# Optimization experiments

Hardware: AMD Instinct MI355X
Metric: run time of the kernel (lower is better)

Reference implementation:

```python
import jax, jax.numpy as jnp
import numpy as np

NUM_WORDS = 10000
IN_DIM = 300
SIZE = 256
NUM_SEQ = 2
B = 16
L = 128
NUM_BASE_LEMMAS = 3000


def _lstm(x, Wi, Wh, b):
    # x: [L, B, D] -> hidden states [L, B, H]
    Bb = x.shape[1]
    H = Wh.shape[0]
    def step(carry, xt):
        h, c = carry
        z = xt @ Wi + h @ Wh + b  # [B, 4H], gate order i,f,g,o (torch convention)
        i, f, g, o = jnp.split(z, 4, axis=-1)
        c = jax.nn.sigmoid(f) * c + jax.nn.sigmoid(i) * jnp.tanh(g)
        h = jax.nn.sigmoid(o) * jnp.tanh(c)
        return (h, c), h
    init = (jnp.zeros((Bb, H), x.dtype), jnp.zeros((Bb, H), x.dtype))
    _, hs = jax.lax.scan(step, init, x)
    return hs


def _bilstm(x, lengths, Wi_f, Wh_f, b_f, Wi_b, Wh_b, b_b):
    # x: [B, L, D]; variable-length bidirectional LSTM, concat outputs [B, L, 2H]
    Bb, Ll, _ = x.shape
    t = jnp.arange(Ll)
    # reverse the valid prefix of each row; padding stays in place
    rev_idx = jnp.where(t[None, :] < lengths[:, None], lengths[:, None] - 1 - t[None, :], t[None, :])
    x_rev = jnp.take_along_axis(x, rev_idx[:, :, None], axis=1)
    hf = _lstm(jnp.swapaxes(x, 0, 1), Wi_f, Wh_f, b_f)
    hb = _lstm(jnp.swapaxes(x_rev, 0, 1), Wi_b, Wh_b, b_b)
    hf = jnp.swapaxes(hf, 0, 1)
    hb = jnp.take_along_axis(jnp.swapaxes(hb, 0, 1), rev_idx[:, :, None], axis=1)
    return jnp.concatenate([hf, hb], axis=-1)


def setup_inputs() -> dict:
    key = jax.random.key(0)
    ks = jax.random.split(key, 16)
    d = {}
    d['word_embeddings'] = jax.random.normal(ks[0], (NUM_WORDS, IN_DIM), jnp.float32)
    # embedding projection Linear(IN_DIM, SIZE)
    d['Wp'] = jax.random.normal(ks[1], (IN_DIM, SIZE), jnp.float32) * 0.05
    d['bp'] = jnp.zeros((SIZE,), jnp.float32)
    D = SIZE + NUM_SEQ
    d['Wi_f'] = jax.random.normal(ks[2], (D, 4 * SIZE), jnp.float32) * 0.05
    d['Wh_f'] = jax.random.normal(ks[3], (SIZE, 4 * SIZE), jnp.float32) * 0.05
    d['b_f'] = jnp.zeros((4 * SIZE,), jnp.float32)
    d['Wi_b'] = jax.random.normal(ks[4], (D, 4 * SIZE), jnp.float32) * 0.05
    d['Wh_b'] = jax.random.normal(ks[5], (SIZE, 4 * SIZE), jnp.float32) * 0.05
    d['b_b'] = jnp.zeros((4 * SIZE,), jnp.float32)
    # encoded projection Linear(2*SIZE, SIZE)
    d['Wenc'] = jax.random.normal(ks[6], (2 * SIZE, SIZE), jnp.float32) * 0.05
    d['benc'] = jnp.zeros((SIZE,), jnp.float32)
    # gate projection Linear(2*SIZE, SIZE), bias init 1.0 per source
    d['Wgate'] = jax.random.normal(ks[7], (2 * SIZE, SIZE), jnp.float32) * 0.05
    d['bgate'] = jnp.ones((SIZE,), jnp.float32)
    d['seq0'] = jax.random.randint(ks[8], (B, L), 0, NUM_WORDS, jnp.int32)
    d['seq1'] = jax.random.randint(ks[9], (B, L), 0, NUM_WORDS, jnp.int32)
    d['len0'] = jax.random.randint(ks[10], (B,), 1, L + 1, jnp.int32)
    d['len1'] = jax.random.randint(ks[11], (B,), 1, L + 1, jnp.int32)
    d['u2l'] = jax.random.randint(ks[12], (NUM_WORDS,), 0, NUM_BASE_LEMMAS, jnp.int32)
    return d


def reference(word_embeddings, Wp, bp, Wi_f, Wh_f, b_f, Wi_b, Wh_b, b_b, Wenc, benc, Wgate, bgate, seq0, seq1, len0, len1, u2l):
    num_words = word_embeddings.shape[0]
    batch = seq0.shape[0]
    size = Wp.shape[1]
    we = jax.nn.relu(word_embeddings @ Wp + bp)  # [num_words, size]
    offsets = jnp.arange(batch, dtype=jnp.int32) * num_words  # [B]
    u2l_off = (u2l[None, :] + offsets[:, None]).reshape(-1)  # [B*num_words]
    num_lemmas = batch * num_words
    ctxt = jnp.tile(we, (batch, 1))  # [B*num_words, size]
    for i, (seq, lengths) in enumerate(((seq0, len0), (seq1, len1))):
        Ll = seq.shape[1]
        seq_off = seq + offsets[:, None]  # [B, L]
        enc_in = ctxt[seq_off]  # gather: [B, L, size]
        mode = jnp.zeros((batch, Ll, NUM_SEQ), enc_in.dtype).at[:, :, i].set(1.0)
        enc_in = jnp.concatenate([enc_in, mode], axis=-1)  # [B, L, size+num_seq]
        h = _bilstm(enc_in, lengths, Wi_f, Wh_f, b_f, Wi_b, Wh_b, b_b)  # [B, L, 2*size]
        enc = h @ Wenc + benc  # [B, L, size]
        mask = (jnp.arange(Ll)[None, :] < lengths[:, None]).astype(enc.dtype)
        enc = enc * mask[:, :, None]
        seq_lemmas = u2l_off[seq_off.reshape(-1)]  # [B*L]
        new_lemma = jax.ops.segment_max(enc.reshape(-1, size), seq_lemmas, num_segments=num_lemmas)
        new_lemma = jax.nn.relu(new_lemma)  # empty segments (-inf) -> 0
        new_word = new_lemma[u2l_off]  # scatter-back via gather: [B*num_words, size]
        gate = jax.nn.sigmoid(jnp.concatenate([ctxt, new_word], axis=-1) @ Wgate + bgate)
        ctxt = ctxt * gate + (1.0 - gate) * new_word
    return ctxt
```

## Files before the change

kernel.cpp:

```cpp
#include <hip/hip_runtime.h>

#define NW    10000
#define INDIM 300
#define SZ    256
#define BB    16
#define LL    128
#define NLEM  3000
#define FH    1024
#define NCAP  8192

typedef short  bf16x8 __attribute__((ext_vector_type(8)));
typedef float  f32x4  __attribute__((ext_vector_type(4)));

__device__ __forceinline__ float sigf(float x){
  return __builtin_amdgcn_rcpf(1.f+__builtin_amdgcn_exp2f(-1.442695041f*x));
}
__device__ __forceinline__ float tanhf_(float x){
  return fmaf(-2.f, __builtin_amdgcn_rcpf(1.f+__builtin_amdgcn_exp2f(2.885390082f*x)), 1.f);
}
__device__ __forceinline__ short f2b(float f){
  unsigned u=__float_as_uint(f); u += 0x7FFFu + ((u>>16)&1u); return (short)(u>>16);
}
__device__ __forceinline__ int pack2(float a, float b){
  return ((int)(unsigned short)f2b(a)) | (((int)(unsigned short)f2b(b))<<16);
}
#define B2F(s) __uint_as_float(((unsigned)(unsigned short)(s))<<16)
#define MFA(a,b,c) __builtin_amdgcn_mfma_f32_16x16x32_bf16(a,b,c,0,0,0)

__global__ void k_we(const float* __restrict__ emb, const float* __restrict__ Wp,
                     const float* __restrict__ bp, float* __restrict__ we){
  __shared__ __align__(16) float As[16][INDIM];
  int r0 = blockIdx.x*16, tid = threadIdx.x;
  for(int i=tid;i<16*INDIM;i+=256){int lr=i/INDIM,d=i-lr*INDIM;
    As[lr][d]=emb[(long)(r0+lr)*INDIM+d];}
  __syncthreads();
  int cl=tid&63, rg=tid>>6;
  float acc[4][4];
  #pragma unroll
  for(int i=0;i<4;i++){acc[i][0]=acc[i][1]=acc[i][2]=acc[i][3]=0.f;}
  for(int k=0;k<INDIM;k+=4){
    float4 a4[4];
    #pragma unroll
    for(int i=0;i<4;i++) a4[i]=*(const float4*)&As[rg*4+i][k];
    #pragma unroll
    for(int j=0;j<4;j++){
      const float* wr=Wp+(long)(k+j)*SZ+cl;
      float w0=wr[0],w1=wr[64],w2=wr[128],w3=wr[192];
      #pragma unroll
      for(int i=0;i<4;i++){
        float a=(j==0)?a4[i].x:(j==1)?a4[i].y:(j==2)?a4[i].z:a4[i].w;
        acc[i][0]=fmaf(a,w0,acc[i][0]);acc[i][1]=fmaf(a,w1,acc[i][1]);
        acc[i][2]=fmaf(a,w2,acc[i][2]);acc[i][3]=fmaf(a,w3,acc[i][3]);
      }
    }
  }
  #pragma unroll
  for(int i=0;i<4;i++){
    int r=r0+rg*4+i;
    #pragma unroll
    for(int cc=0;cc<4;cc++){int col=cl+cc*64;
      we[(long)r*SZ+col]=fmaxf(acc[i][cc]+bp[col],0.f);}
  }
}

__global__ void k_prep(const float* __restrict__ Wh_f, const float* __restrict__ Wh_b,
                       short* __restrict__ frag){
  int tid = blockIdx.x*256 + threadIdx.x;
  int l=tid&63, f=(tid>>6)&63, w=(tid>>12)&7, dir=tid>>15;
  const float* Wh = dir? Wh_b : Wh_f;
  int ks=f&7, T2=f>>3, s2=T2>>2, g=T2&3;
  int col = g*256 + w*32 + s2*16 + (l&15);
  int k0  = ks*32 + (l>>4)*8;
  short v[8];
  #pragma unroll
  for(int j=0;j<8;j++) v[j]=f2b(Wh[(long)(k0+j)*FH + col]);
  *(bf16x8*)(frag + (long)tid*8) = *(bf16x8*)v;
}

__global__ void k_prepwi(const float* __restrict__ Wi_f, const float* __restrict__ Wi_b,
                         short* __restrict__ wf){
  int tid = blockIdx.x*256 + threadIdx.x;
  int l=tid&63, ks=(tid>>6)&7, ct=(tid>>9)&63, dir=tid>>15;
  const float* Wi = dir? Wi_b : Wi_f;
  int col = ct*16 + (l&15);
  int k0  = ks*32 + (l>>4)*8;
  short v[8];
  #pragma unroll
  for(int j=0;j<8;j++) v[j]=f2b(Wi[(long)(k0+j)*FH + col]);
  *(bf16x8*)(wf + (long)tid*8) = *(bf16x8*)v;
}

__global__ void k_prepenc(const float* __restrict__ Wenc, short* __restrict__ wef){
  int tid = blockIdx.x*256 + threadIdx.x;
  int l=tid&63, ks=(tid>>6)&15, ct=tid>>10;
  int col = ct*16 + (l&15);
  int k0  = ks*32 + (l>>4)*8;
  short v[8];
  #pragma unroll
  for(int j=0;j<8;j++) v[j]=f2b(Wenc[(long)(k0+j)*SZ + col]);
  *(bf16x8*)(wef + (long)tid*8) = *(bf16x8*)v;
}

__global__ void k_xwi_mfma(const int* __restrict__ seq, const int* __restrict__ len,
                      const float* __restrict__ srcw, long bstride,
                      const float* __restrict__ ctxtT, const int* __restrict__ idxmap,
                      const float* __restrict__ Wi_f, const float* __restrict__ bvf,
                      const float* __restrict__ Wi_b, const float* __restrict__ bvb,
                      const short* __restrict__ wf, int iseq, short* __restrict__ xwo){
  __shared__ __align__(16) short As[64*264];
  __shared__ const float* rowp[64];
  int bx=blockIdx.x, dir=bx>>5, blk=bx&31, tid=threadIdx.x;
  int w=tid>>6, l=tid&63;
  if(tid<64){
    int t = blk*4 + (tid>>4), b = tid&15;
    int lb=len[b];
    int tt=(dir==0)? t : ((t<lb)? (lb-1-t) : t);
    int tok=seq[b*LL+tt];
    const float* rp;
    if(idxmap){
      int im=idxmap[b*NW+tok];
      rp = (im>=0)? ctxtT+(long)im*SZ : srcw+(long)tok*SZ;
    }else{
      rp = srcw + (long)b*bstride + (long)tok*SZ;
    }
    rowp[tid]=rp;
  }
  __syncthreads();
  for(int i2=tid;i2<64*64;i2+=256){
    int lr=i2>>6, c4=(i2&63)*4;
    float4 v=*(const float4*)(rowp[lr]+c4);
    int2 pk; pk.x=pack2(v.x,v.y); pk.y=pack2(v.z,v.w);
    *(int2*)&As[lr*264+c4]=pk;
  }
  __syncthreads();
  const float* __restrict__ Wi = dir? Wi_b : Wi_f;
  const float* __restrict__ bv = dir? bvb : bvf;
  const short* wfd = wf + (long)dir*262144;
  for(int n2=0;n2<16;n2++){
    int ct = w*16 + n2;
    const short* bfp = wfd + ((long)ct*8)*512 + l*8;
    f32x4 Z={0.f,0.f,0.f,0.f};
    f32x4 C0=Z,C1=Z,C2=Z,C3=Z;
    #pragma unroll
    for(int ks=0;ks<8;ks++){
      bf16x8 bb=*(const bf16x8*)(bfp + ks*512);
      int ao = ks*32 + (l>>4)*8;
      bf16x8 a0=*(const bf16x8*)(&As[((l&15)    )*264 + ao]);
      bf16x8 a1=*(const bf16x8*)(&As[((l&15)+16 )*264 + ao]);
      bf16x8 a2=*(const bf16x8*)(&As[((l&15)+32 )*264 + ao]);
      bf16x8 a3=*(const bf16x8*)(&As[((l&15)+48 )*264 + ao]);
      C0=MFA(a0,bb,C0); C1=MFA(a1,bb,C1); C2=MFA(a2,bb,C2); C3=MFA(a3,bb,C3);
    }
    int g=ct>>4, w2=(ct&15)>>1, s2=ct&1;
    int col = g*256 + w2*32 + s2*16 + (l&15);
    float be = Wi[(long)(SZ+iseq)*FH+col] + bv[col];
    #pragma unroll
    for(int m=0;m<4;m++){
      f32x4 Cm = (m==0)?C0:(m==1)?C1:(m==2)?C2:C3;
      long base=((((long)dir*128 + blk*4 + m)*8 + w2)*64 + (l>>4)*16 + (l&15))*32
                + s2*16 + g*4;
      int2 pk; pk.x=pack2(Cm[0]+be,Cm[1]+be); pk.y=pack2(Cm[2]+be,Cm[3]+be);
      *(int2*)(xwo+base)=pk;
    }
  }
}

#define LDFW(f)    (*(const bf16x8*)(fr + (long)(f)*512 + l*8))
#define LDLW(i2,ks) (*(const bf16x8*)(bl + ((i2)*8+(ks))*512 + l*8))
#define DECLWT(T) bf16x8 W##T##_0=LDFW((T)*8+0),W##T##_1=LDFW((T)*8+1),W##T##_2=LDFW((T)*8+2),W##T##_3=LDFW((T)*8+3),W##T##_4=LDFW((T)*8+4),W##T##_5=LDFW((T)*8+5),W##T##_6=LDFW((T)*8+6),W##T##_7=LDFW((T)*8+7);
#define MMRT(T,Cv) { Cv=MFA(A0,W##T##_0,Cv); Cv=MFA(A1,W##T##_1,Cv); Cv=MFA(A2,W##T##_2,Cv); Cv=MFA(A3,W##T##_3,Cv); Cv=MFA(A4,W##T##_4,Cv); Cv=MFA(A5,W##T##_5,Cv); Cv=MFA(A6,W##T##_6,Cv); Cv=MFA(A7,W##T##_7,Cv); }
#define MMLT(i2,Cv) { Cv=MFA(A0,LDLW(i2,0),Cv); Cv=MFA(A1,LDLW(i2,1),Cv); Cv=MFA(A2,LDLW(i2,2),Cv); Cv=MFA(A3,LDLW(i2,3),Cv); Cv=MFA(A4,LDLW(i2,4),Cv); Cv=MFA(A5,LDLW(i2,5),Cv); Cv=MFA(A6,LDLW(i2,6),Cv); Cv=MFA(A7,LDLW(i2,7),Cv); }
#define MMST(Cv) { Cv=MFA(A0,S0,Cv); Cv=MFA(A1,S1,Cv); Cv=MFA(A2,S2,Cv); Cv=MFA(A3,S3,Cv); Cv=MFA(A4,S4,Cv); Cv=MFA(A5,S5,Cv); Cv=MFA(A6,S6,Cv); Cv=MFA(A7,S7,Cv); }
#define LOADST(f0) S0=LDFW((f0)+0); S1=LDFW((f0)+1); S2=LDFW((f0)+2); S3=LDFW((f0)+3); S4=LDFW((f0)+4); S5=LDFW((f0)+5); S6=LDFW((f0)+6); S7=LDFW((f0)+7);
#define G1(s,r,CA,CB,CC,CD,XA,XB) { \
  float zi=CA[r]+B2F(XA[r]), zf=CB[r]+B2F(XA[4+(r)]), zg=CC[r]+B2F(XB[r]), zo=CD[r]+B2F(XB[4+(r)]); \
  cst_##s##_##r = sigf(zf)*cst_##s##_##r + sigf(zi)*tanhf_(zg); \
  float hv = sigf(zo)*tanhf_(cst_##s##_##r); \
  int b_=4*(l>>4)+(r); int u_=w*32+(s)*16+(l&15); \
  hbn[b_*264+u_]=f2b(hv); }
#define GP(s,CA,CB,CC,CD,XA,XB) \
  G1(s,0,CA,CB,CC,CD,XA,XB) G1(s,1,CA,CB,CC,CD,XA,XB) \
  G1(s,2,CA,CB,CC,CD,XA,XB) G1(s,3,CA,CB,CC,CD,XA,XB)

extern __shared__ char smem_raw[];

__global__ __launch_bounds__(512,2) void k_lstm_w8(
    const short* __restrict__ frag, const short* __restrict__ xq,
    short* __restrict__ hgs){
  const int dir=blockIdx.x, tid=threadIdx.x, w=tid>>6, l=tid&63;
  short* hb=(short*)smem_raw;
  short* bl=(short*)(smem_raw+16896)+w*8192;
  const short* fr = frag + (long)(dir*8+w)*32768;
  for(int i=tid;i<4224;i+=512) ((int*)smem_raw)[i]=0;
  #pragma unroll
  for(int c2=0;c2<16;c2++)
    *(f32x4*)(bl+c2*512+l*8) = *(const f32x4*)(fr+(long)(32+c2)*512+l*8);
  DECLWT(0) DECLWT(1) DECLWT(2) DECLWT(3)
  float cst_0_0=0,cst_0_1=0,cst_0_2=0,cst_0_3=0,
        cst_1_0=0,cst_1_1=0,cst_1_2=0,cst_1_3=0;
  __syncthreads();
  const short* xwb = xq + ((long)dir*128*8 + w)*2048 + (long)l*32;
  short* hgb = hgs + (long)dir*524288;
  const int db=tid>>5, du=(tid&31)*8;
  bf16x8 S0,S1,S2,S3,S4,S5,S6,S7;
  for(int t=0;t<LL;t++){
    const int cur=t&1, nxt=cur^1;
    LOADST(48)
    const short* xp = xwb + (long)t*16384;
    bf16x8 X0=*(const bf16x8*)(xp+0), X1=*(const bf16x8*)(xp+8);
    const short* hr = hb + cur*4224 + (l&15)*264 + (l>>4)*8;
    bf16x8 A0=*(const bf16x8*)(hr+0),   A1=*(const bf16x8*)(hr+32),
           A2=*(const bf16x8*)(hr+64),  A3=*(const bf16x8*)(hr+96),
           A4=*(const bf16x8*)(hr+128), A5=*(const bf16x8*)(hr+160),
           A6=*(const bf16x8*)(hr+192), A7=*(const bf16x8*)(hr+224);
    f32x4 Z={0.f,0.f,0.f,0.f};
    f32x4 C00=Z,C01=Z,C02=Z,C03=Z,C10=Z,C11=Z,C12=Z,C13=Z;
    MMRT(0,C00) MMRT(1,C01) MMRT(2,C02) MMRT(3,C03)
    MMLT(0,C10) MMLT(1,C11)
    MMST(C12)
    LOADST(56)
    bf16x8 X2=*(const bf16x8*)(xp+16), X3=*(const bf16x8*)(xp+24);
    short* hbn = hb + nxt*4224;
    GP(0, C00,C01,C02,C03, X0,X1)
    MMST(C13)
    GP(1, C10,C11,C12,C13, X2,X3)
    __syncthreads();
    f32x4 hv4 = *(const f32x4*)(hbn + db*264 + du);
    *(f32x4*)(hgb + ((long)t*16 + db)*256 + du) = hv4;
  }
}

__global__ void k_enc_mfma(const int* __restrict__ seq, const int* __restrict__ len,
                      const int* __restrict__ u2l, const short* __restrict__ hgs,
                      const short* __restrict__ wef, const float* __restrict__ benc,
                      unsigned int* __restrict__ lembuf, unsigned int* __restrict__ flags){
  __shared__ __align__(16) short As[64*520];
  __shared__ const short* pf16[64]; __shared__ const short* pb16[64];
  __shared__ int lem_s[64], val_s[64], b_s[64];
  int r0=blockIdx.x*64, tid=threadIdx.x, w=tid>>6, l=tid&63;
  if(tid<64){
    int r=r0+tid, b=r>>7, t=r&127, lb=len[b];
    int v=(t<lb); val_s[tid]=v; b_s[tid]=b;
    int lem=u2l[seq[r]]; lem_s[tid]=lem;
    pf16[tid]=hgs+((long)t*BB+b)*SZ;
    int tr=v? (lb-1-t) : t;
    pb16[tid]=hgs+((long)(LL+tr)*BB+b)*SZ;
    if(v) flags[(long)b*NLEM+lem]=1u;
  }
  __syncthreads();
  for(int i2=tid;i2<64*128;i2+=256){
    int lr=i2>>7, cc=(i2&127)*4;
    const short* sp=(cc<256)? pf16[lr]+cc : pb16[lr]+(cc-256);
    *(int2*)&As[lr*520+cc]=*(const int2*)sp;
  }
  __syncthreads();
  for(int n2=0;n2<4;n2++){
    int ct=w*4+n2;
    f32x4 Z={0.f,0.f,0.f,0.f};
    f32x4 C0=Z,C1=Z,C2=Z,C3=Z;
    #pragma unroll
    for(int ks=0;ks<16;ks++){
      bf16x8 bb=*(const bf16x8*)(wef+((long)(ct*16+ks))*512+l*8);
      int ao=ks*32+(l>>4)*8;
      bf16x8 a0=*(const bf16x8*)(&As[((l&15)    )*520+ao]);
      bf16x8 a1=*(const bf16x8*)(&As[((l&15)+16 )*520+ao]);
      bf16x8 a2=*(const bf16x8*)(&As[((l&15)+32 )*520+ao]);
      bf16x8 a3=*(const bf16x8*)(&As[((l&15)+48 )*520+ao]);
      C0=MFA(a0,bb,C0); C1=MFA(a1,bb,C1); C2=MFA(a2,bb,C2); C3=MFA(a3,bb,C3);
    }
    int col=ct*16+(l&15);
    float be=benc[col];
    #pragma unroll
    for(int m=0;m<4;m++){
      f32x4 Cm=(m==0)?C0:(m==1)?C1:(m==2)?C2:C3;
      #pragma unroll
      for(int reg=0;reg<4;reg++){
        int row=m*16+(l>>4)*4+reg;
        if(val_s[row]){
          float e=fmaxf(Cm[reg]+be,0.f);
          atomicMax(&lembuf[((long)b_s[row]*NLEM+lem_s[row])*SZ+col], __float_as_uint(e));
        }
      }
    }
  }
}

__global__ void k_rowgemm(const float* __restrict__ A, const float* __restrict__ W,
                          float* __restrict__ C, const unsigned int* __restrict__ flags){
  __shared__ __align__(16) float As[16][SZ];
  __shared__ int any_s;
  int r0=blockIdx.x*16, tid=threadIdx.x;
  if(tid==0){
    int a = flags? 0 : 1;
    if(flags){ for(int i=0;i<16;i++) a |= (int)flags[r0+i]; }
    any_s=a;
  }
  __syncthreads();
  if(!any_s) return;
  for(int i=tid;i<16*SZ;i+=256){int lr=i>>8,j=i&(SZ-1);As[lr][j]=A[(long)(r0+lr)*SZ+j];}
  __syncthreads();
  int cl=tid&63, rg=tid>>6;
  float acc[4][4];
  #pragma unroll
  for(int i=0;i<4;i++){acc[i][0]=acc[i][1]=acc[i][2]=acc[i][3]=0.f;}
  for(int k=0;k<SZ;k+=4){
    float4 a4[4];
    #pragma unroll
    for(int i=0;i<4;i++) a4[i]=*(const float4*)&As[rg*4+i][k];
    #pragma unroll
    for(int j=0;j<4;j++){
      const float* wr=W+(long)(k+j)*SZ+cl;
      float w0=wr[0],w1=wr[64],w2=wr[128],w3=wr[192];
      #pragma unroll
      for(int i=0;i<4;i++){
        float a=(j==0)?a4[i].x:(j==1)?a4[i].y:(j==2)?a4[i].z:a4[i].w;
        acc[i][0]=fmaf(a,w0,acc[i][0]);acc[i][1]=fmaf(a,w1,acc[i][1]);
        acc[i][2]=fmaf(a,w2,acc[i][2]);acc[i][3]=fmaf(a,w3,acc[i][3]);
      }
    }
  }
  #pragma unroll
  for(int i=0;i<4;i++){
    int r=r0+rg*4+i;
    #pragma unroll
    for(int cc=0;cc<4;cc++) C[(long)r*SZ+cl+cc*64]=acc[i][cc];
  }
}

__global__ void k_rowgemm_n(const float* __restrict__ A, const float* __restrict__ W,
                            float* __restrict__ C, const int* __restrict__ cnt, int ncap){
  __shared__ __align__(16) float As[16][SZ];
  int n=*cnt; if(n>ncap)n=ncap;
  int r0=blockIdx.x*16, tid=threadIdx.x;
  if(r0>=n) return;
  for(int i=tid;i<16*SZ;i+=256){int lr=i>>8,j=i&(SZ-1);
    As[lr][j]= (r0+lr<n)? A[(long)(r0+lr)*SZ+j] : 0.f;}
  __syncthreads();
  int cl=tid&63, rg=tid>>6;
  float acc[4][4];
  #pragma unroll
  for(int i=0;i<4;i++){acc[i][0]=acc[i][1]=acc[i][2]=acc[i][3]=0.f;}
  for(int k=0;k<SZ;k+=4){
    float4 a4[4];
    #pragma unroll
    for(int i=0;i<4;i++) a4[i]=*(const float4*)&As[rg*4+i][k];
    #pragma unroll
    for(int j=0;j<4;j++){
      const float* wr=W+(long)(k+j)*SZ+cl;
      float w0=wr[0],w1=wr[64],w2=wr[128],w3=wr[192];
      #pragma unroll
      for(int i=0;i<4;i++){
        float a=(j==0)?a4[i].x:(j==1)?a4[i].y:(j==2)?a4[i].z:a4[i].w;
        acc[i][0]=fmaf(a,w0,acc[i][0]);acc[i][1]=fmaf(a,w1,acc[i][1]);
        acc[i][2]=fmaf(a,w2,acc[i][2]);acc[i][3]=fmaf(a,w3,acc[i][3]);
      }
    }
  }
  #pragma unroll
  for(int i=0;i<4;i++){
    int r=r0+rg*4+i;
    if(r<n){
      #pragma unroll
      for(int cc=0;cc<4;cc++) C[(long)r*SZ+cl+cc*64]=acc[i][cc];
    }
  }
}

__global__ void k_compact(const int* __restrict__ u2l, const unsigned int* __restrict__ flags,
                          int* __restrict__ cnt, int* __restrict__ list,
                          int* __restrict__ idxmap, int ncap){
  int r = blockIdx.x*256+threadIdx.x;
  if(r>=BB*NW) return;
  int b=r/NW, w=r-b*NW;
  int im=-1;
  if(flags[(long)b*NLEM+u2l[w]]){
    int idx=atomicAdd(cnt,1);
    if(idx<ncap){ list[idx]=r; im=idx; }
  }
  idxmap[r]=im;
}

__global__ void k_gate0c(const float* __restrict__ we, const float* __restrict__ P0,
                         const float* __restrict__ Q, const float* __restrict__ lembuf,
                         const int* __restrict__ u2l, const float* __restrict__ bg,
                         const int* __restrict__ cnt, const int* __restrict__ list,
                         float* __restrict__ ctxtT, int ncap){
  int n=*cnt; if(n>ncap)n=ncap;
  long idx=(long)blockIdx.x*256+threadIdx.x;
  long i=idx>>6; int k4=(int)(idx&63);
  if(i>=n) return;
  int r=list[i]; int b=r/NW, w=r-b*NW;
  int lem=u2l[w];
  long qb=((long)b*NLEM+lem)*SZ;
  float4 p =((const float4*)(P0+(long)w*SZ))[k4];
  float4 wv=((const float4*)(we+(long)w*SZ))[k4];
  float4 bgv=((const float4*)bg)[k4];
  float4 q =((const float4*)(Q+qb))[k4];
  float4 nw=((const float4*)(lembuf+qb))[k4];
  float4 o;
  { float g=sigf(p.x+q.x+bgv.x); o.x=wv.x*g+(1.f-g)*nw.x; }
  { float g=sigf(p.y+q.y+bgv.y); o.y=wv.y*g+(1.f-g)*nw.y; }
  { float g=sigf(p.z+q.z+bgv.z); o.z=wv.z*g+(1.f-g)*nw.z; }
  { float g=sigf(p.w+q.w+bgv.w); o.w=wv.w*g+(1.f-g)*nw.w; }
  ((float4*)ctxtT)[i*64+k4]=o;
}

__global__ void k_base0ip(float* __restrict__ we, const float* __restrict__ P0,
                          const float* __restrict__ bg){
  long idx=(long)blockIdx.x*256+threadIdx.x;
  if(idx>=(long)NW*SZ/4) return;
  int k4=(int)(idx&63);
  float4 wv=((float4*)we)[idx];
  float4 p =((const float4*)P0)[idx];
  float4 bgv=((const float4*)bg)[k4];
  wv.x*=sigf(p.x+bgv.x); wv.y*=sigf(p.y+bgv.y);
  wv.z*=sigf(p.z+bgv.z); wv.w*=sigf(p.w+bgv.w);
  ((float4*)we)[idx]=wv;
}

__global__ void k_gate0(const float* __restrict__ we, const float* __restrict__ P0,
                        const float* __restrict__ Q, const float* __restrict__ lembuf,
                        const int* __restrict__ u2l, const unsigned int* __restrict__ flags,
                        const float* __restrict__ bg, float* __restrict__ out){
  long idx=(long)blockIdx.x*256+threadIdx.x;
  const long TOTAL4=(long)BB*NW*SZ/4;
  if(idx>=TOTAL4) return;
  long row=idx>>6; int k4=(int)(idx&63);
  int r32=(int)row;
  int b=r32/NW, w=r32-b*NW;
  int lem=u2l[w];
  long qb=((long)b*NLEM+lem)*SZ;
  unsigned int fl=flags[(long)b*NLEM+lem];
  float4 p =((const float4*)(P0+(long)w*SZ))[k4];
  float4 wv=((const float4*)(we+(long)w*SZ))[k4];
  float4 bgv=((const float4*)bg)[k4];
  float4 q, nw;
  if(fl){ q=((const float4*)(Q+qb))[k4]; nw=((const float4*)(lembuf+qb))[k4]; }
  else  { q=make_float4(0.f,0.f,0.f,0.f); nw=q; }
  float4 o;
  { float g=sigf(p.x+q.x+bgv.x); o.x=wv.x*g+(1.f-g)*nw.x; }
  { float g=sigf(p.y+q.y+bgv.y); o.y=wv.y*g+(1.f-g)*nw.y; }
  { float g=sigf(p.z+q.z+bgv.z); o.z=wv.z*g+(1.f-g)*nw.z; }
  { float g=sigf(p.w+q.w+bgv.w); o.w=wv.w*g+(1.f-g)*nw.w; }
  ((float4*)out)[idx]=o;
}

__global__ void k_gate1e(const float* __restrict__ base0, const float* __restrict__ ctxtT,
                         const float* __restrict__ P1b, const float* __restrict__ Pt,
                         const int* __restrict__ idxmap,
                         const float* __restrict__ Q, const float* __restrict__ lembuf,
                         const int* __restrict__ u2l, const unsigned int* __restrict__ flags,
                         const float* __restrict__ bg, float* __restrict__ out){
  long idx=(long)blockIdx.x*256+threadIdx.x;
  const long TOTAL4=(long)BB*NW*SZ/4;
  if(idx>=TOTAL4) return;
  long row=idx>>6; int k4=(int)(idx&63);
  int r32=(int)row;
  int b=r32/NW, w=r32-b*NW;
  int im=idxmap[r32];
  int lem=u2l[w];
  long qb=((long)b*NLEM+lem)*SZ;
  unsigned int fl=flags[(long)b*NLEM+lem];
  float4 p, cv;
  if(im>=0){ p=((const float4*)(Pt+(long)im*SZ))[k4]; cv=((const float4*)(ctxtT+(long)im*SZ))[k4]; }
  else     { p=((const float4*)(P1b+(long)w*SZ))[k4]; cv=((const float4*)(base0+(long)w*SZ))[k4]; }
  float4 bgv=((const float4*)bg)[k4];
  float4 q, nw;
  if(fl){ q=((const float4*)(Q+qb))[k4]; nw=((const float4*)(lembuf+qb))[k4]; }
  else  { q=make_float4(0.f,0.f,0.f,0.f); nw=q; }
  float4 o;
  { float g=sigf(p.x+q.x+bgv.x); o.x=cv.x*g+(1.f-g)*nw.x; }
  { float g=sigf(p.y+q.y+bgv.y); o.y=cv.y*g+(1.f-g)*nw.y; }
  { float g=sigf(p.z+q.z+bgv.z); o.z=cv.z*g+(1.f-g)*nw.z; }
  { float g=sigf(p.w+q.w+bgv.w); o.w=cv.w*g+(1.f-g)*nw.w; }
  ((float4*)out)[idx]=o;
}

__global__ void k_gate1(const float* __restrict__ ctxt, const float* __restrict__ Wg,
                        const float* __restrict__ Q, const float* __restrict__ lembuf,
                        const int* __restrict__ u2l, const unsigned int* __restrict__ flags,
                        const float* __restrict__ bg, float* __restrict__ out){
  __shared__ __align__(16) float As[64][SZ];
  __shared__ __align__(16) float Ws[64][SZ];
  __shared__ int lem_s[64];
  int r0=blockIdx.x*64, tid=threadIdx.x;
  for(int i=tid;i<64*SZ;i+=256){int lr=i>>8,j=i&(SZ-1);
    As[lr][j]=ctxt[(long)(r0+lr)*SZ+j];}
  if(tid<64){int r=r0+tid; lem_s[tid]=u2l[r%NW];}
  int cl=tid&63, rg=tid>>6;
  float acc[16][4];
  #pragma unroll
  for(int i=0;i<16;i++){acc[i][0]=acc[i][1]=acc[i][2]=acc[i][3]=0.f;}
  for(int kb=0;kb<4;kb++){
    __syncthreads();
    for(int i=tid;i<64*SZ;i+=256){int lr=i>>8,j=i&(SZ-1);
      Ws[lr][j]=Wg[(long)(kb*64+lr)*SZ+j];}
    __syncthreads();
    for(int k=0;k<64;k+=4){
      float4 a4[16];
      #pragma unroll
      for(int i=0;i<16;i++) a4[i]=*(const float4*)&As[rg*16+i][kb*64+k];
      #pragma unroll
      for(int j=0;j<4;j++){
        float w0=Ws[k+j][cl],w1=Ws[k+j][cl+64],w2=Ws[k+j][cl+128],w3=Ws[k+j][cl+192];
        #pragma unroll
        for(int i=0;i<16;i++){
          float a=(j==0)?a4[i].x:(j==1)?a4[i].y:(j==2)?a4[i].z:a4[i].w;
          acc[i][0]=fmaf(a,w0,acc[i][0]);acc[i][1]=fmaf(a,w1,acc[i][1]);
          acc[i][2]=fmaf(a,w2,acc[i][2]);acc[i][3]=fmaf(a,w3,acc[i][3]);
        }
      }
    }
  }
  #pragma unroll
  for(int i=0;i<16;i++){
    int lr=rg*16+i, r=r0+lr, b=r/NW;
    long base=((long)b*NLEM+lem_s[lr])*SZ;
    unsigned int fl=flags[(long)b*NLEM+lem_s[lr]];
    #pragma unroll
    for(int cc=0;cc<4;cc++){
      int col=cl+cc*64;
      float qv=0.f, nw=0.f;
      if(fl){ qv=Q[base+col]; nw=lembuf[base+col]; }
      float g=sigf(acc[i][cc]+qv+bg[col]);
      out[(long)r*SZ+col]=As[lr][col]*g+(1.f-g)*nw;
    }
  }
}

extern "C" void kernel_launch(void* const* d_in, const int* in_sizes, int n_in,
                              void* d_out, int out_size, void* d_ws, size_t ws_size,
                              hipStream_t stream){
  const float* emb  =(const float*)d_in[0];
  const float* Wp   =(const float*)d_in[1];
  const float* bp   =(const float*)d_in[2];
  const float* Wi_f =(const float*)d_in[3];
  const float* Wh_f =(const float*)d_in[4];
  const float* b_f  =(const float*)d_in[5];
  const float* Wi_b =(const float*)d_in[6];
  const float* Wh_b =(const float*)d_in[7];
  const float* b_b  =(const float*)d_in[8];
  const float* Wenc =(const float*)d_in[9];
  const float* benc =(const float*)d_in[10];
  const float* Wg   =(const float*)d_in[11];
  const float* bg   =(const float*)d_in[12];
  const int*   seq0 =(const int*)d_in[13];
  const int*   seq1 =(const int*)d_in[14];
  const int*   len0 =(const int*)d_in[15];
  const int*   len1 =(const int*)d_in[16];
  const int*   u2l  =(const int*)d_in[17];

  float* ws    = (float*)d_ws;
  float* we    = ws;
  float* xwi   = we    + 2560000;
  float* ctxtT = xwi   + 2097152;
  float* hglob = xwi   + 4194304;
  float* lembuf= hglob + 1048576;
  float* flags = lembuf+ 12288000;
  float* Q     = flags + 48000;
  float* P0    = Q     + 12288000;
  short* whb   = (short*)(P0 + 2560000);
  short* wifrag= whb + 524288;
  short* wefrag= wifrag + 524288;
  int*   idxmap= (int*)(P0 + 2560000 + 262144 + 262144 + 65536);
  int*   list  = idxmap + 160000;
  int*   cnt   = list + NCAP;
  float* Ptouch= (float*)(cnt + 4);
  long base_floats = (long)(Ptouch - ws);
  long avail = ((long)(ws_size/4) - base_floats)/SZ;
  int sparse_ok = (avail >= NCAP);
  float* out   = (float*)d_out;

  hipFuncSetAttribute((const void*)k_lstm_w8,
                      hipFuncAttributeMaxDynamicSharedMemorySize, 147968);

  k_we<<<NW/16,256,0,stream>>>(emb,Wp,bp,we);
  k_rowgemm<<<NW/16,256,0,stream>>>(we,Wg,P0,nullptr);
  k_prep<<<256,256,0,stream>>>(Wh_f,Wh_b,whb);
  k_prepwi<<<256,256,0,stream>>>(Wi_f,Wi_b,wifrag);
  k_prepenc<<<64,256,0,stream>>>(Wenc,wefrag);

  hipMemsetAsync(lembuf,0,(size_t)(12288000+48000)*4,stream);
  k_xwi_mfma<<<64,256,0,stream>>>(seq0,len0,we,0L,nullptr,nullptr,
                                  Wi_f,b_f,Wi_b,b_b,wifrag,0,(short*)xwi);
  k_lstm_w8<<<2,512,147968,stream>>>(whb,(const short*)xwi,(short*)hglob);
  k_enc_mfma<<<BB*LL/64,256,0,stream>>>(seq0,len0,u2l,(const short*)hglob,wefrag,benc,
                                        (unsigned int*)lembuf,(unsigned int*)flags);
  k_rowgemm<<<BB*NLEM/16,256,0,stream>>>(lembuf,Wg+(long)SZ*SZ,Q,
                                         (const unsigned int*)flags);
  if(sparse_ok){
    hipMemsetAsync(cnt,0,4,stream);
    k_compact<<<(BB*NW+255)/256,256,0,stream>>>(u2l,(const unsigned int*)flags,
                                                cnt,list,idxmap,NCAP);
    k_gate0c<<<NCAP*64/256,256,0,stream>>>(we,P0,Q,lembuf,u2l,bg,cnt,list,ctxtT,NCAP);
    k_rowgemm_n<<<NCAP/16,256,0,stream>>>(ctxtT,Wg,Ptouch,cnt,NCAP);
    k_base0ip<<<(NW*SZ/4+255)/256,256,0,stream>>>(we,P0,bg);
    k_rowgemm<<<NW/16,256,0,stream>>>(we,Wg,P0,nullptr);
  }else{
    long nb=((long)BB*NW*SZ/4+255)/256;
    k_gate0<<<(int)nb,256,0,stream>>>(we,P0,Q,lembuf,u2l,
                                      (const unsigned int*)flags,bg,out);
  }

  hipMemsetAsync(lembuf,0,(size_t)(12288000+48000)*4,stream);
  if(sparse_ok){
    k_xwi_mfma<<<64,256,0,stream>>>(seq1,len1,we,0L,ctxtT,idxmap,
                                    Wi_f,b_f,Wi_b,b_b,wifrag,1,(short*)xwi);
  }else{
    k_xwi_mfma<<<64,256,0,stream>>>(seq1,len1,out,(long)NW*SZ,nullptr,nullptr,
                                    Wi_f,b_f,Wi_b,b_b,wifrag,1,(short*)xwi);
  }
  k_lstm_w8<<<2,512,147968,stream>>>(whb,(const short*)xwi,(short*)hglob);
  k_enc_mfma<<<BB*LL/64,256,0,stream>>>(seq1,len1,u2l,(const short*)hglob,wefrag,benc,
                                        (unsigned int*)lembuf,(unsigned int*)flags);
  k_rowgemm<<<BB*NLEM/16,256,0,stream>>>(lembuf,Wg+(long)SZ*SZ,Q,
                                         (const unsigned int*)flags);
  if(sparse_ok){
    long nb=((long)BB*NW*SZ/4+255)/256;
    k_gate1e<<<(int)nb,256,0,stream>>>(we,ctxtT,P0,Ptouch,idxmap,Q,lembuf,u2l,
                                       (const unsigned int*)flags,bg,out);
  }else{
    k_gate1<<<BB*NW/64,256,0,stream>>>(out,Wg,Q,lembuf,u2l,
                                       (const unsigned int*)flags,bg,out);
  }
}
```

Before: 1.346 ms.

## Run independent row GEMMs as extra blocks inside the LSTM kernel launch

The recurrent LSTM kernel uses only two blocks, so the GPU sits mostly idle while it runs. This change appends extra blocks to that launch which compute the word-gate projection `we@Wg` into P0 and the compacted `ctxtT@Wg` into Ptouch, replacing the separate `k_rowgemm` and `k_rowgemm_n` launches. It also moves the P0 recompute that followed `k_base0ip` into the second LSTM launch. The GEMM blocks use a 64-row tile with 512 threads and inherit the LSTM kernel's large dynamic LDS allocation, and they may compete with the LSTM blocks for memory bandwidth.

```diff
diff --git a/kernel.cpp b/kernel.cpp
--- a/kernel.cpp
+++ b/kernel.cpp
@@ -165,6 +165,45 @@
   }
 }
 
+__device__ __forceinline__ void rowgemm64(const float* __restrict__ A,
+                                          const float* __restrict__ W,
+                                          float* __restrict__ C,
+                                          int n, int r0, int tid, float* Asf){
+  for(int i=tid;i<64*SZ;i+=512){
+    int lr=i>>8; int r=r0+lr;
+    Asf[i]= (r<n)? A[(long)r*SZ+(i&255)] : 0.f;
+  }
+  __syncthreads();
+  int cl=tid&63, rg=tid>>6;
+  float acc[8][4];
+  #pragma unroll
+  for(int i=0;i<8;i++){acc[i][0]=acc[i][1]=acc[i][2]=acc[i][3]=0.f;}
+  for(int k=0;k<SZ;k+=4){
+    float4 a4[8];
+    #pragma unroll
+    for(int i=0;i<8;i++) a4[i]=*(const float4*)&Asf[(rg*8+i)*SZ+k];
+    #pragma unroll
+    for(int j=0;j<4;j++){
+      const float* wr=W+(long)(k+j)*SZ+cl;
+      float w0=wr[0],w1=wr[64],w2=wr[128],w3=wr[192];
+      #pragma unroll
+      for(int i=0;i<8;i++){
+        float a=(j==0)?a4[i].x:(j==1)?a4[i].y:(j==2)?a4[i].z:a4[i].w;
+        acc[i][0]=fmaf(a,w0,acc[i][0]);acc[i][1]=fmaf(a,w1,acc[i][1]);
+        acc[i][2]=fmaf(a,w2,acc[i][2]);acc[i][3]=fmaf(a,w3,acc[i][3]);
+      }
+    }
+  }
+  #pragma unroll
+  for(int i=0;i<8;i++){
+    int r=r0+rg*8+i;
+    if(r<n){
+      #pragma unroll
+      for(int cc=0;cc<4;cc++) C[(long)r*SZ+cl+cc*64]=acc[i][cc];
+    }
+  }
+}
+
 #define LDFW(f)    (*(const bf16x8*)(fr + (long)(f)*512 + l*8))
 #define LDLW(i2,ks) (*(const bf16x8*)(bl + ((i2)*8+(ks))*512 + l*8))
 #define DECLWT(T) bf16x8 W##T##_0=LDFW((T)*8+0),W##T##_1=LDFW((T)*8+1),W##T##_2=LDFW((T)*8+2),W##T##_3=LDFW((T)*8+3),W##T##_4=LDFW((T)*8+4),W##T##_5=LDFW((T)*8+5),W##T##_6=LDFW((T)*8+6),W##T##_7=LDFW((T)*8+7);
@@ -184,10 +223,27 @@
 
 extern __shared__ char smem_raw[];
 
-__global__ __launch_bounds__(512,2) void k_lstm_w8(
+__global__ __launch_bounds__(512,2) void k_lstm_f(
     const short* __restrict__ frag, const short* __restrict__ xq,
-    short* __restrict__ hgs){
-  const int dir=blockIdx.x, tid=threadIdx.x, w=tid>>6, l=tid&63;
+    short* __restrict__ hgs,
+    const float* __restrict__ gA1, const float* __restrict__ gW1,
+    float* __restrict__ gC1, int n1,
+    const float* __restrict__ gA2, const float* __restrict__ gW2,
+    float* __restrict__ gC2, const int* __restrict__ cnt2, int ncap2){
+  const int bid=blockIdx.x, tid=threadIdx.x;
+  if(bid>=2){
+    float* Asf=(float*)smem_raw;
+    int nb1=(n1+63)>>6;
+    int gb=bid-2;
+    if(gb<nb1){ rowgemm64(gA1,gW1,gC1,n1,gb*64,tid,Asf); }
+    else if(cnt2){
+      int n2=*cnt2; if(n2>ncap2)n2=ncap2;
+      int r0=(gb-nb1)*64;
+      if(r0<n2) rowgemm64(gA2,gW2,gC2,n2,r0,tid,Asf);
+    }
+    return;
+  }
+  const int dir=bid, w=tid>>6, l=tid&63;
   short* hb=(short*)smem_raw;
   short* bl=(short*)(smem_raw+16896)+w*8192;
   const short* fr = frag + (long)(dir*8+w)*32768;
@@ -324,45 +380,6 @@
     int r=r0+rg*4+i;
     #pragma unroll
     for(int cc=0;cc<4;cc++) C[(long)r*SZ+cl+cc*64]=acc[i][cc];
-  }
-}
-
-__global__ void k_rowgemm_n(const float* __restrict__ A, const float* __restrict__ W,
-                            float* __restrict__ C, const int* __restrict__ cnt, int ncap){
-  __shared__ __align__(16) float As[16][SZ];
-  int n=*cnt; if(n>ncap)n=ncap;
-  int r0=blockIdx.x*16, tid=threadIdx.x;
-  if(r0>=n) return;
-  for(int i=tid;i<16*SZ;i+=256){int lr=i>>8,j=i&(SZ-1);
-    As[lr][j]= (r0+lr<n)? A[(long)(r0+lr)*SZ+j] : 0.f;}
-  __syncthreads();
-  int cl=tid&63, rg=tid>>6;
-  float acc[4][4];
-  #pragma unroll
-  for(int i=0;i<4;i++){acc[i][0]=acc[i][1]=acc[i][2]=acc[i][3]=0.f;}
-  for(int k=0;k<SZ;k+=4){
-    float4 a4[4];
-    #pragma unroll
-    for(int i=0;i<4;i++) a4[i]=*(const float4*)&As[rg*4+i][k];
-    #pragma unroll
-    for(int j=0;j<4;j++){
-      const float* wr=W+(long)(k+j)*SZ+cl;
-      float w0=wr[0],w1=wr[64],w2=wr[128],w3=wr[192];
-      #pragma unroll
-      for(int i=0;i<4;i++){
-        float a=(j==0)?a4[i].x:(j==1)?a4[i].y:(j==2)?a4[i].z:a4[i].w;
-        acc[i][0]=fmaf(a,w0,acc[i][0]);acc[i][1]=fmaf(a,w1,acc[i][1]);
-        acc[i][2]=fmaf(a,w2,acc[i][2]);acc[i][3]=fmaf(a,w3,acc[i][3]);
-      }
-    }
-  }
-  #pragma unroll
-  for(int i=0;i<4;i++){
-    int r=r0+rg*4+i;
-    if(r<n){
-      #pragma unroll
-      for(int cc=0;cc<4;cc++) C[(long)r*SZ+cl+cc*64]=acc[i][cc];
-    }
   }
 }
 
@@ -571,19 +588,22 @@
   int sparse_ok = (avail >= NCAP);
   float* out   = (float*)d_out;
 
-  hipFuncSetAttribute((const void*)k_lstm_w8,
+  hipFuncSetAttribute((const void*)k_lstm_f,
                       hipFuncAttributeMaxDynamicSharedMemorySize, 147968);
 
   k_we<<<NW/16,256,0,stream>>>(emb,Wp,bp,we);
-  k_rowgemm<<<NW/16,256,0,stream>>>(we,Wg,P0,nullptr);
   k_prep<<<256,256,0,stream>>>(Wh_f,Wh_b,whb);
   k_prepwi<<<256,256,0,stream>>>(Wi_f,Wi_b,wifrag);
   k_prepenc<<<64,256,0,stream>>>(Wenc,wefrag);
 
+  const int NB1=(NW+63)/64;
+
   hipMemsetAsync(lembuf,0,(size_t)(12288000+48000)*4,stream);
   k_xwi_mfma<<<64,256,0,stream>>>(seq0,len0,we,0L,nullptr,nullptr,
                                   Wi_f,b_f,Wi_b,b_b,wifrag,0,(short*)xwi);
-  k_lstm_w8<<<2,512,147968,stream>>>(whb,(const short*)xwi,(short*)hglob);
+  k_lstm_f<<<2+NB1,512,147968,stream>>>(whb,(const short*)xwi,(short*)hglob,
+                                        we,Wg,P0,NW,
+                                        nullptr,nullptr,nullptr,nullptr,0);
   k_enc_mfma<<<BB*LL/64,256,0,stream>>>(seq0,len0,u2l,(const short*)hglob,wefrag,benc,
                                         (unsigned int*)lembuf,(unsigned int*)flags);
   k_rowgemm<<<BB*NLEM/16,256,0,stream>>>(lembuf,Wg+(long)SZ*SZ,Q,
@@ -593,9 +613,7 @@
     k_compact<<<(BB*NW+255)/256,256,0,stream>>>(u2l,(const unsigned int*)flags,
                                                 cnt,list,idxmap,NCAP);
     k_gate0c<<<NCAP*64/256,256,0,stream>>>(we,P0,Q,lembuf,u2l,bg,cnt,list,ctxtT,NCAP);
-    k_rowgemm_n<<<NCAP/16,256,0,stream>>>(ctxtT,Wg,Ptouch,cnt,NCAP);
     k_base0ip<<<(NW*SZ/4+255)/256,256,0,stream>>>(we,P0,bg);
-    k_rowgemm<<<NW/16,256,0,stream>>>(we,Wg,P0,nullptr);
   }else{
     long nb=((long)BB*NW*SZ/4+255)/256;
     k_gate0<<<(int)nb,256,0,stream>>>(we,P0,Q,lembuf,u2l,
@@ -606,11 +624,16 @@
   if(sparse_ok){
     k_xwi_mfma<<<64,256,0,stream>>>(seq1,len1,we,0L,ctxtT,idxmap,
                                     Wi_f,b_f,Wi_b,b_b,wifrag,1,(short*)xwi);
+    k_lstm_f<<<2+NB1+NCAP/64,512,147968,stream>>>(whb,(const short*)xwi,(short*)hglob,
+                                                  we,Wg,P0,NW,
+                                                  ctxtT,Wg,Ptouch,cnt,NCAP);
   }else{
     k_xwi_mfma<<<64,256,0,stream>>>(seq1,len1,out,(long)NW*SZ,nullptr,nullptr,
                                     Wi_f,b_f,Wi_b,b_b,wifrag,1,(short*)xwi);
-  }
-  k_lstm_w8<<<2,512,147968,stream>>>(whb,(const short*)xwi,(short*)hglob);
+    k_lstm_f<<<2,512,147968,stream>>>(whb,(const short*)xwi,(short*)hglob,
+                                      nullptr,nullptr,nullptr,0,
+                                      nullptr,nullptr,nullptr,nullptr,0);
+  }
   k_enc_mfma<<<BB*LL/64,256,0,stream>>>(seq1,len1,u2l,(const short*)hglob,wefrag,benc,
                                         (unsigned int*)lembuf,(unsigned int*)flags);
   k_rowgemm<<<BB*NLEM/16,256,0,stream>>>(lembuf,Wg+(long)SZ*SZ,Q,
```

Measured after the change: 1.264 ms. -6.1%, faster.
